# Kernel tuning notes

Measured on AMD Instinct MI355X. Metric: run time of the kernel, lower is better.

## Reference

```python
import jax, jax.numpy as jnp
import numpy as np

B, S, D_IN, D_OUT = 4, 4096, 2048, 2048
NUM_ADAPTERS, RANK = 8, 16


def setup_inputs() -> dict:
    key = jax.random.key(0)
    ks = jax.random.split(key, 7)
    x = jax.random.normal(ks[0], (B, S, D_IN), dtype=jnp.float32)
    # adapter ids per token in [0, NUM_ADAPTERS]; 0 means 'no adapter'
    lora_mapping = jax.random.randint(ks[1], (B * S,), 0, NUM_ADAPTERS + 1, dtype=jnp.int32)
    weight = jax.random.normal(ks[2], (D_OUT, D_IN), dtype=jnp.float32) * (D_IN ** -0.5)
    bias = jax.random.normal(ks[3], (D_OUT,), dtype=jnp.float32) * 0.01
    # stacked adapters: aid a (1-indexed in mapping) lives at row a-1
    lora_a = jax.random.normal(ks[4], (NUM_ADAPTERS, RANK, D_IN), dtype=jnp.float32) * (D_IN ** -0.5)
    lora_b = jax.random.normal(ks[5], (NUM_ADAPTERS, D_OUT, RANK), dtype=jnp.float32) * (RANK ** -0.5)
    scaling = jnp.full((NUM_ADAPTERS,), 2.0, dtype=jnp.float32)
    return {"x": x, "lora_mapping": lora_mapping, "weight": weight, "bias": bias,
            "lora_a": lora_a, "lora_b": lora_b, "scaling": scaling}


def reference(x, lora_mapping, weight, bias, lora_a, lora_b, scaling):
    # Base dense linear: res = x @ W^T + b
    res = jnp.einsum('bsd,od->bso', x, weight) + bias  # [B,S,D_OUT]
    n_adapters = lora_a.shape[0]
    x2 = x.reshape(-1, x.shape[-1])                    # [N, D_IN]
    # one_hot(aid-1): aid==0 maps to -1 -> all-zero row (adapter skipped),
    # matching the torch loop that ignores aid 0. Fold scaling in here.
    sel = jax.nn.one_hot(lora_mapping - 1, n_adapters, dtype=x.dtype) * scaling  # [N, A]
    # Batched gather-matmul-scatter expressed as dense-over-adapters einsum:
    # u[n,a,r] = x[n] @ la[a]^T ; masked/scaled by sel ; delta[n] = sum_a u[n,a] @ lb[a]^T
    u = jnp.einsum('nd,ard->nar', x2, lora_a) * sel[..., None]  # [N, A, R]
    delta = jnp.einsum('nar,aor->no', u, lora_b)                # [N, D_OUT]
    return res + delta.reshape(res.shape)
```

## Files before the change

kernel.cpp:

```cpp
#include <hip/hip_runtime.h>
#include <hip/hip_bf16.h>


#define D_IN   2048
#define D_OUT  2048
#define NTOK   16384
#define RANK   16
#define NADAPT 8
#define KEXT   2176
#define BM     128
#define BN     128
#define BK     64

typedef __attribute__((ext_vector_type(8))) __bf16 bf16x8;
typedef __attribute__((ext_vector_type(8))) unsigned short u16x8;
typedef __attribute__((ext_vector_type(4))) float  f32x4;

__device__ inline unsigned short f2bf(float f) {
    unsigned u = __builtin_bit_cast(unsigned, f);
    u += 0x7fffu + ((u >> 16) & 1u);
    return (unsigned short)(u >> 16);
}

__global__ void conv_la(const float4* __restrict__ la, ushort4* __restrict__ La) {
    int t = blockIdx.x * 256 + threadIdx.x;
    float4 v = la[t];
    ushort4 s;
    s.x = f2bf(v.x); s.y = f2bf(v.y); s.z = f2bf(v.z); s.w = f2bf(v.w);
    La[t] = s;
}

__global__ void prep_x_mfma(const float* __restrict__ x, const int* __restrict__ map,
                            const unsigned short* __restrict__ La,
                            const float* __restrict__ scaling,
                            unsigned short* __restrict__ Xe) {
    int t = threadIdx.x, lane = t & 63, wave = t >> 6;
    int n0 = blockIdx.x * 16;
    int crow = t >> 4;
    int ckc  = t & 15;
    int arow = lane & 15;
    int kq   = lane >> 4;

    f32x4 acc[2] = {};

    const float* xrow_c = x + (size_t)(n0 + crow) * D_IN + ckc * 2;
    unsigned short* xo_c = Xe + (size_t)(n0 + crow) * KEXT + ckc * 2;
    const float* xrow_a = x + (size_t)(n0 + arow) * D_IN + kq * 8;
    const unsigned short* lb0 = La + (size_t)(wave * 32 + arow) * D_IN + kq * 8;
    const unsigned short* lb1 = lb0 + (size_t)16 * D_IN;

    for (int k0 = 0; k0 < D_IN; k0 += 32) {
        float2 cv = *(const float2*)(xrow_c + k0);
        ushort2 cs; cs.x = f2bf(cv.x); cs.y = f2bf(cv.y);
        *(ushort2*)(xo_c + k0) = cs;
        float4 a0 = *(const float4*)(xrow_a + k0);
        float4 a1 = *(const float4*)(xrow_a + k0 + 4);
        u16x8 au;
        au[0] = f2bf(a0.x); au[1] = f2bf(a0.y); au[2] = f2bf(a0.z); au[3] = f2bf(a0.w);
        au[4] = f2bf(a1.x); au[5] = f2bf(a1.y); au[6] = f2bf(a1.z); au[7] = f2bf(a1.w);
        bf16x8 af = __builtin_bit_cast(bf16x8, au);
        bf16x8 b0 = *(const bf16x8*)(lb0 + k0);
        bf16x8 b1 = *(const bf16x8*)(lb1 + k0);
        acc[0] = __builtin_amdgcn_mfma_f32_16x16x32_bf16(af, b0, acc[0], 0, 0, 0);
        acc[1] = __builtin_amdgcn_mfma_f32_16x16x32_bf16(af, b1, acc[1], 0, 0, 0);
    }

    int aid_m[4];
#pragma unroll
    for (int r = 0; r < 4; ++r) aid_m[r] = map[n0 + kq * 4 + r];
#pragma unroll
    for (int j = 0; j < 2; ++j) {
        int c = wave * 32 + j * 16 + arow;
        int a = c >> 4;
        float sc = scaling[a];
#pragma unroll
        for (int r = 0; r < 4; ++r) {
            int token = n0 + kq * 4 + r;
            unsigned short v = 0;
            if (aid_m[r] == a + 1) v = f2bf(acc[j][r] * sc);
            Xe[(size_t)token * KEXT + D_IN + c] = v;
        }
    }
}

__global__ void prep_w(const float4* __restrict__ w, const float* __restrict__ lora_b,
                       unsigned short* __restrict__ We) {
    int wave = threadIdx.x >> 6, lane = threadIdx.x & 63;
    int o = blockIdx.x * 4 + wave;
    const float4* wr = w + (size_t)o * (D_IN / 4);
    unsigned short* wo = We + (size_t)o * KEXT;
#pragma unroll
    for (int j = 0; j < 8; ++j) {
        float4 v = wr[j * 64 + lane];
        ushort4 s;
        s.x = f2bf(v.x); s.y = f2bf(v.y); s.z = f2bf(v.z); s.w = f2bf(v.w);
        *(ushort4*)(wo + (j * 64 + lane) * 4) = s;
    }
    int c0 = lane * 2;
    int a = c0 >> 4, r = c0 & 15;
    const float* src = lora_b + ((size_t)a * D_OUT + o) * RANK + r;
    ushort2 e; e.x = f2bf(src[0]); e.y = f2bf(src[1]);
    *(ushort2*)(wo + D_IN + c0) = e;
}

__global__ void gemm_fused(const unsigned short* __restrict__ Xe,
                           const unsigned short* __restrict__ We,
                           const float* __restrict__ bias,
                           float* __restrict__ out) {
    __shared__ unsigned short As[BM * BK];
    __shared__ unsigned short Bs[BN * BK];

    int t = threadIdx.x;
    int lane = t & 63, wave = t >> 6;
    int g = blockIdx.x;
    int group = g >> 7, within = g & 127;
    int bm = group * 8 + (within & 7);
    int bn = within >> 3;

    int wm = wave >> 1, wn = wave & 1;
    f32x4 acc[4][4] = {};

    for (int k0 = 0; k0 < KEXT; k0 += BK) {
        __syncthreads();
#pragma unroll
        for (int c = 0; c < 4; ++c) {
            int linear = (wave * 4 + c) * 64 + lane;
            int row = linear >> 3;
            int kc  = linear & 7;
            int gc  = kc ^ (row & 7);
            const unsigned short* ga = Xe + (size_t)(bm * BM + row) * KEXT + k0 + gc * 8;
            __builtin_amdgcn_global_load_lds(
                (const __attribute__((address_space(1))) unsigned int*)ga,
                (__attribute__((address_space(3))) unsigned int*)(As + (wave * 4 + c) * 512),
                16, 0, 0);
            const unsigned short* gb = We + (size_t)(bn * BN + row) * KEXT + k0 + gc * 8;
            __builtin_amdgcn_global_load_lds(
                (const __attribute__((address_space(1))) unsigned int*)gb,
                (__attribute__((address_space(3))) unsigned int*)(Bs + (wave * 4 + c) * 512),
                16, 0, 0);
        }
        __syncthreads();
#pragma unroll
        for (int ks = 0; ks < 2; ++ks) {
            bf16x8 af[4], bfr[4];
            int gchunk = ks * 4 + (lane >> 4);
            int sw = gchunk ^ (lane & 7);
#pragma unroll
            for (int i = 0; i < 4; ++i) {
                int rowA = wm * 64 + i * 16 + (lane & 15);
                af[i]  = *(const bf16x8*)(As + rowA * BK + sw * 8);
                int rowB = wn * 64 + i * 16 + (lane & 15);
                bfr[i] = *(const bf16x8*)(Bs + rowB * BK + sw * 8);
            }
#pragma unroll
            for (int i = 0; i < 4; ++i)
#pragma unroll
                for (int j = 0; j < 4; ++j)
                    acc[i][j] = __builtin_amdgcn_mfma_f32_16x16x32_bf16(af[i], bfr[j], acc[i][j], 0, 0, 0);
        }
    }

    int colq = lane & 15, rq = lane >> 4;
#pragma unroll
    for (int j = 0; j < 4; ++j) {
        int col = bn * BN + wn * 64 + j * 16 + colq;
        float bv = bias[col];
#pragma unroll
        for (int i = 0; i < 4; ++i) {
            int row0 = bm * BM + wm * 64 + i * 16 + rq * 4;
#pragma unroll
            for (int r = 0; r < 4; ++r)
                out[(size_t)(row0 + r) * D_OUT + col] = acc[i][j][r] + bv;
        }
    }
}

extern "C" void kernel_launch(void* const* d_in, const int* in_sizes, int n_in,
                              void* d_out, int out_size, void* d_ws, size_t ws_size,
                              hipStream_t stream) {
    (void)in_sizes; (void)n_in; (void)out_size; (void)ws_size;
    const float* x       = (const float*)d_in[0];
    const int*   map     = (const int*)d_in[1];
    const float* weight  = (const float*)d_in[2];
    const float* bias    = (const float*)d_in[3];
    const float* lora_a  = (const float*)d_in[4];
    const float* lora_b  = (const float*)d_in[5];
    const float* scaling = (const float*)d_in[6];
    float* out = (float*)d_out;

    unsigned short* Xe = (unsigned short*)d_ws;
    unsigned short* We = Xe + (size_t)NTOK * KEXT;
    unsigned short* La = We + (size_t)D_OUT * KEXT;

    conv_la<<<256, 256, 0, stream>>>((const float4*)lora_a, (ushort4*)La);
    prep_x_mfma<<<NTOK / 16, 256, 0, stream>>>(x, map, La, scaling, Xe);
    prep_w<<<D_OUT / 4, 256, 0, stream>>>((const float4*)weight, lora_b, We);
    gemm_fused<<<(NTOK / BM) * (D_OUT / BN), 256, 0, stream>>>(Xe, We, bias, out);
}
```

Baseline: 456.2 us.

## Split prep into bulk bf16 conversion and separate LoRA-A projection kernels

Replaces the fused per-token prep kernel and the weight prep kernel with one grid-stride kernel that converts x and W to bf16 together using 16-byte stores, a small kernel that writes the lora_b extension columns, and a separate MFMA kernel that computes the scaled LoRA-A projection from the already converted bf16 x. The aim is better memory coalescing and larger vector accesses during conversion, and avoiding a second fp32 read of x for the projection. The cost is an extra kernel launch and a re-read of the bf16 x from global memory.

```diff
diff --git a/kernel.cpp b/kernel.cpp
--- a/kernel.cpp
+++ b/kernel.cpp
@@ -11,6 +11,7 @@
 #define BM     128
 #define BN     128
 #define BK     64
+#define NROWS  (NTOK + D_OUT)
 
 typedef __attribute__((ext_vector_type(8))) __bf16 bf16x8;
 typedef __attribute__((ext_vector_type(8))) unsigned short u16x8;
@@ -30,77 +31,67 @@
     La[t] = s;
 }
 
-__global__ void prep_x_mfma(const float* __restrict__ x, const int* __restrict__ map,
-                            const unsigned short* __restrict__ La,
-                            const float* __restrict__ scaling,
-                            unsigned short* __restrict__ Xe) {
+__global__ void conv_all(const float* __restrict__ x, const float* __restrict__ w,
+                         unsigned short* __restrict__ XeWe) {
+    const size_t TOTAL = (size_t)NROWS * (D_IN / 8);
+    size_t stride = (size_t)gridDim.x * blockDim.x;
+    for (size_t u = (size_t)blockIdx.x * blockDim.x + threadIdx.x; u < TOTAL; u += stride) {
+        int n  = (int)(u >> 8);
+        int kc = ((int)u & 255) * 8;
+        const float* src = (n < NTOK) ? x + (size_t)n * D_IN + kc
+                                      : w + (size_t)(n - NTOK) * D_IN + kc;
+        float4 v0 = *(const float4*)(src);
+        float4 v1 = *(const float4*)(src + 4);
+        u16x8 s;
+        s[0] = f2bf(v0.x); s[1] = f2bf(v0.y); s[2] = f2bf(v0.z); s[3] = f2bf(v0.w);
+        s[4] = f2bf(v1.x); s[5] = f2bf(v1.y); s[6] = f2bf(v1.z); s[7] = f2bf(v1.w);
+        *(u16x8*)(XeWe + (size_t)n * KEXT + kc) = s;
+    }
+}
+
+__global__ void ext_w(const float* __restrict__ lora_b, unsigned short* __restrict__ We) {
+    int t = blockIdx.x * 256 + threadIdx.x;
+    int o = t >> 7, c = t & 127;
+    int a = c >> 4, r = c & 15;
+    We[(size_t)o * KEXT + D_IN + c] = f2bf(lora_b[((size_t)a * D_OUT + o) * RANK + r]);
+}
+
+__global__ void ext_mfma(unsigned short* Xe, const int* __restrict__ map,
+                         const unsigned short* __restrict__ La,
+                         const float* __restrict__ scaling) {
     int t = threadIdx.x, lane = t & 63, wave = t >> 6;
-    int n0 = blockIdx.x * 16;
-    int crow = t >> 4;
-    int ckc  = t & 15;
+    int n0 = blockIdx.x * 32;
     int arow = lane & 15;
     int kq   = lane >> 4;
 
     f32x4 acc[2] = {};
 
-    const float* xrow_c = x + (size_t)(n0 + crow) * D_IN + ckc * 2;
-    unsigned short* xo_c = Xe + (size_t)(n0 + crow) * KEXT + ckc * 2;
-    const float* xrow_a = x + (size_t)(n0 + arow) * D_IN + kq * 8;
-    const unsigned short* lb0 = La + (size_t)(wave * 32 + arow) * D_IN + kq * 8;
-    const unsigned short* lb1 = lb0 + (size_t)16 * D_IN;
+    const unsigned short* xr0 = Xe + (size_t)(n0 + arow) * KEXT + kq * 8;
+    const unsigned short* xr1 = xr0 + (size_t)16 * KEXT;
+    const unsigned short* lb  = La + (size_t)(wave * 16 + arow) * D_IN + kq * 8;
 
+#pragma unroll 4
     for (int k0 = 0; k0 < D_IN; k0 += 32) {
-        float2 cv = *(const float2*)(xrow_c + k0);
-        ushort2 cs; cs.x = f2bf(cv.x); cs.y = f2bf(cv.y);
-        *(ushort2*)(xo_c + k0) = cs;
-        float4 a0 = *(const float4*)(xrow_a + k0);
-        float4 a1 = *(const float4*)(xrow_a + k0 + 4);
-        u16x8 au;
-        au[0] = f2bf(a0.x); au[1] = f2bf(a0.y); au[2] = f2bf(a0.z); au[3] = f2bf(a0.w);
-        au[4] = f2bf(a1.x); au[5] = f2bf(a1.y); au[6] = f2bf(a1.z); au[7] = f2bf(a1.w);
-        bf16x8 af = __builtin_bit_cast(bf16x8, au);
-        bf16x8 b0 = *(const bf16x8*)(lb0 + k0);
-        bf16x8 b1 = *(const bf16x8*)(lb1 + k0);
-        acc[0] = __builtin_amdgcn_mfma_f32_16x16x32_bf16(af, b0, acc[0], 0, 0, 0);
-        acc[1] = __builtin_amdgcn_mfma_f32_16x16x32_bf16(af, b1, acc[1], 0, 0, 0);
+        bf16x8 a0 = *(const bf16x8*)(xr0 + k0);
+        bf16x8 a1 = *(const bf16x8*)(xr1 + k0);
+        bf16x8 b  = *(const bf16x8*)(lb + k0);
+        acc[0] = __builtin_amdgcn_mfma_f32_16x16x32_bf16(a0, b, acc[0], 0, 0, 0);
+        acc[1] = __builtin_amdgcn_mfma_f32_16x16x32_bf16(a1, b, acc[1], 0, 0, 0);
     }
 
-    int aid_m[4];
+    int colq = lane & 15, rq = lane >> 4;
+    int c = wave * 16 + colq;
+    float sc = scaling[wave];
 #pragma unroll
-    for (int r = 0; r < 4; ++r) aid_m[r] = map[n0 + kq * 4 + r];
-#pragma unroll
-    for (int j = 0; j < 2; ++j) {
-        int c = wave * 32 + j * 16 + arow;
-        int a = c >> 4;
-        float sc = scaling[a];
+    for (int i = 0; i < 2; ++i) {
 #pragma unroll
         for (int r = 0; r < 4; ++r) {
-            int token = n0 + kq * 4 + r;
+            int token = n0 + i * 16 + rq * 4 + r;
             unsigned short v = 0;
-            if (aid_m[r] == a + 1) v = f2bf(acc[j][r] * sc);
+            if (map[token] == wave + 1) v = f2bf(acc[i][r] * sc);
             Xe[(size_t)token * KEXT + D_IN + c] = v;
         }
     }
-}
-
-__global__ void prep_w(const float4* __restrict__ w, const float* __restrict__ lora_b,
-                       unsigned short* __restrict__ We) {
-    int wave = threadIdx.x >> 6, lane = threadIdx.x & 63;
-    int o = blockIdx.x * 4 + wave;
-    const float4* wr = w + (size_t)o * (D_IN / 4);
-    unsigned short* wo = We + (size_t)o * KEXT;
-#pragma unroll
-    for (int j = 0; j < 8; ++j) {
-        float4 v = wr[j * 64 + lane];
-        ushort4 s;
-        s.x = f2bf(v.x); s.y = f2bf(v.y); s.z = f2bf(v.z); s.w = f2bf(v.w);
-        *(ushort4*)(wo + (j * 64 + lane) * 4) = s;
-    }
-    int c0 = lane * 2;
-    int a = c0 >> 4, r = c0 & 15;
-    const float* src = lora_b + ((size_t)a * D_OUT + o) * RANK + r;
-    ushort2 e; e.x = f2bf(src[0]); e.y = f2bf(src[1]);
-    *(ushort2*)(wo + D_IN + c0) = e;
 }
 
 __global__ void gemm_fused(const unsigned short* __restrict__ Xe,
@@ -193,7 +184,8 @@
     unsigned short* La = We + (size_t)D_OUT * KEXT;
 
     conv_la<<<256, 256, 0, stream>>>((const float4*)lora_a, (ushort4*)La);
-    prep_x_mfma<<<NTOK / 16, 256, 0, stream>>>(x, map, La, scaling, Xe);
-    prep_w<<<D_OUT / 4, 256, 0, stream>>>((const float4*)weight, lora_b, We);
+    conv_all<<<2304, 256, 0, stream>>>(x, weight, Xe);
+    ext_w<<<1024, 256, 0, stream>>>(lora_b, We);
+    ext_mfma<<<NTOK / 32, 512, 0, stream>>>(Xe, map, La, scaling);
     gemm_fused<<<(NTOK / BM) * (D_OUT / BN), 256, 0, stream>>>(Xe, We, bias, out);
 }
```

New measurement: 463.8 us. About the same (+1.7%).
